# Kernel optimization log

Hardware: AMD Instinct MI355X
Metric: run time of the kernel (lower is better)

Reference implementation:

```python
import jax, jax.numpy as jnp
import numpy as np

N, E = 100000, 1600000
IN, H, Z, C = 64, 128, 64, 2


def _glorot(key, fan_in, fan_out):
    s = jnp.sqrt(2.0 / (fan_in + fan_out)).astype(jnp.float32)
    return jax.random.normal(key, (fan_in, fan_out), dtype=jnp.float32) * s


def setup_inputs() -> dict:
    key = jax.random.key(0)
    ks = jax.random.split(key, 16)
    dims = [(IN, H), (H, H), (H, Z), (H, H), (H, Z), (Z, H), (H, H), (H, IN * C)]
    names = ['in', 'mu0', 'mu', 'si0', 'si', 'z', 'd0', 'out']
    inp = {
        'x': jax.random.normal(ks[0], (N, IN), dtype=jnp.float32),
        'eps': jax.random.normal(ks[1], (N, Z), dtype=jnp.float32),
        'edge_index': jax.random.randint(ks[2], (2, E), 0, N, dtype=jnp.int64),
    }
    for i, (nm, (fi, fo)) in enumerate(zip(names, dims)):
        inp[f'w_{nm}'] = _glorot(ks[3 + i], fi, fo)
        inp[f'b_{nm}'] = jnp.zeros((fo,), dtype=jnp.float32)
    return inp


def _gcn(x, W, b, src, dst, dinv):
    # PyG GCNConv: symmetric normalization with self-loops.
    h = x @ W                                      # [N, d_out]
    norm = (dinv[src] * dinv[dst])[:, None]        # [E, 1]
    agg = jax.ops.segment_sum(h[src] * norm, dst, num_segments=N)
    agg = agg + h * (dinv * dinv)[:, None]         # self-loop term (norm = 1/deg)
    return agg + b


def reference(x, edge_index, eps,
              w_in, b_in, w_mu0, b_mu0, w_mu, b_mu,
              w_si0, b_si0, w_si, b_si,
              w_z, b_z, w_d0, b_d0, w_out, b_out):
    src, dst = edge_index[0], edge_index[1]
    deg = jax.ops.segment_sum(jnp.ones((E,), jnp.float32), dst, num_segments=N) + 1.0
    dinv = jax.lax.rsqrt(deg)
    # encode
    h = jax.nn.relu(_gcn(x, w_in, b_in, src, dst, dinv))
    mu = jax.nn.relu(_gcn(h, w_mu0, b_mu0, src, dst, dinv))
    mu = jax.nn.relu(_gcn(mu, w_mu, b_mu, src, dst, dinv))
    si = jax.nn.relu(_gcn(h, w_si0, b_si0, src, dst, dinv))
    si = jax.nn.sigmoid(_gcn(si, w_si, b_si, src, dst, dinv))
    # reparameterize
    z = mu + si * eps
    # decode (first decoder layer has no activation, per the original forward)
    r = _gcn(z, w_z, b_z, src, dst, dinv)
    r = jax.nn.relu(_gcn(r, w_d0, b_d0, src, dst, dinv))
    logits = _gcn(r, w_out, b_out, src, dst, dinv)   # [N, IN*C]
    logits = logits.reshape(-1, C)                   # [N*IN, C]
    return logits, mu, si
```

## Files before the change

### kernel.cpp

```cpp
#include <hip/hip_runtime.h>


typedef short bf16x8 __attribute__((ext_vector_type(8)));
typedef float f32x4 __attribute__((ext_vector_type(4)));

__device__ __forceinline__ ushort f2bf(float f) {
    uint x = __float_as_uint(f);
    uint r = x + 0x7FFFu + ((x >> 16) & 1u);
    return (ushort)(r >> 16);
}
__device__ __forceinline__ float bf2f(ushort h) {
    return __uint_as_float(((uint)h) << 16);
}
__device__ __forceinline__ float dot2bf(uint a, uint b, float c) {
    float d;
    asm("v_dot2_f32_bf16 %0, %1, %2, %3" : "=v"(d) : "v"(a), "v"(b), "v"(c));
    return d;
}

__global__ __launch_bounds__(1024) void counts_kernel(const int* __restrict__ dst,
        int* __restrict__ deg, int* __restrict__ bc0, int E, int NB, int shift) {
    __shared__ int h[8192];
    for (int j = threadIdx.x; j < NB; j += 1024) h[j] = 0;
    __syncthreads();
    int stride = gridDim.x * 1024;
    for (int i = blockIdx.x * 1024 + threadIdx.x; i < E; i += stride) {
        int d = dst[i];
        atomicAdd(&deg[d], 1);
        atomicAdd(&h[d >> shift], 1);
    }
    __syncthreads();
    for (int j = threadIdx.x; j < NB; j += 1024) {
        int v = h[j];
        if (v) atomicAdd(&bc0[j], v);
    }
}

__global__ void dinv_kernel(const int* __restrict__ deg, float* __restrict__ dinv, int N) {
    int i = blockIdx.x * blockDim.x + threadIdx.x;
    if (i < N) dinv[i] = rsqrtf((float)(deg[i] + 1));
}

__global__ __launch_bounds__(1024) void scan_block_kernel(const int* __restrict__ in,
                                                          int* __restrict__ out,
                                                          int* __restrict__ bsum, int n) {
    __shared__ int s[1024];
    int i = blockIdx.x * 1024 + threadIdx.x;
    int v = (i < n) ? in[i] : 0;
    s[threadIdx.x] = v;
    __syncthreads();
    for (int off = 1; off < 1024; off <<= 1) {
        int t = (threadIdx.x >= off) ? s[threadIdx.x - off] : 0;
        __syncthreads();
        s[threadIdx.x] += t;
        __syncthreads();
    }
    if (i < n) out[i] = s[threadIdx.x] - v;
    if (threadIdx.x == 1023) bsum[blockIdx.x] = s[1023];
}

__global__ __launch_bounds__(1024) void scan_partials_kernel(int* __restrict__ bsum, int nb) {
    __shared__ int s[1024];
    int v = (threadIdx.x < nb) ? bsum[threadIdx.x] : 0;
    s[threadIdx.x] = v;
    __syncthreads();
    for (int off = 1; off < 1024; off <<= 1) {
        int t = (threadIdx.x >= off) ? s[threadIdx.x - off] : 0;
        __syncthreads();
        s[threadIdx.x] += t;
        __syncthreads();
    }
    if (threadIdx.x < nb) bsum[threadIdx.x] = s[threadIdx.x] - v;
}

__global__ __launch_bounds__(1024) void scan_add_kernel(int* __restrict__ arr,
                                                        const int* __restrict__ bsum, int n, int total) {
    int i = blockIdx.x * 1024 + threadIdx.x;
    if (i < n) arr[i] += bsum[blockIdx.x];
    if (i == 0) arr[n] = total;
}

__global__ void scatter_kernel(const int* __restrict__ src, const int* __restrict__ dst,
                               const int* __restrict__ bin_start, int* __restrict__ bc1,
                               int2* __restrict__ ebuf, int E, int shift) {
    int i = blockIdx.x * blockDim.x + threadIdx.x;
    if (i < E) {
        int d = dst[i];
        int b = d >> shift;
        int pos = bin_start[b] + atomicAdd(&bc1[b], 1);
        ebuf[pos] = make_int2(src[i], d);
    }
}

__global__ void place2_kernel(const int2* __restrict__ ebuf, const int* __restrict__ row_start,
                              int* __restrict__ cnt, int2* __restrict__ csr,
                              const float* __restrict__ dinv, int E) {
    int i = blockIdx.x * blockDim.x + threadIdx.x;
    if (i < E) {
        int2 e = ebuf[i];
        int pos = row_start[e.y] + atomicAdd(&cnt[e.y], 1);
        csr[pos] = make_int2(e.x, (int)(uint)f2bf(dinv[e.x] * dinv[e.y]));
    }
}

__global__ void rowsum_kernel(const int2* __restrict__ csr, const int* __restrict__ row_start,
                              const float* __restrict__ dinv, float* __restrict__ cvec, int N) {
    int j = blockIdx.x * blockDim.x + threadIdx.x;
    if (j >= N) return;
    float s = dinv[j] * dinv[j];
    int b = row_start[j], e = row_start[j + 1];
    for (int k = b; k < e; ++k) s += bf2f((ushort)((uint)csr[k].y & 0xFFFFu));
    cvec[j] = s;
}

__global__ void wcpack_kernel(const float* __restrict__ w_z, const float* __restrict__ b_z,
                              const float* __restrict__ w_d0,
                              ushort* __restrict__ P_wc, float* __restrict__ bzw) {
    int o = blockIdx.x * 256 + threadIdx.x;
    if (o >= 65 * 128) return;
    int i = o >> 7, j = o & 127;
    float s = 0.f;
    for (int k = 0; k < 128; ++k) {
        float a = (i < 64) ? w_z[i * 128 + k] : b_z[k];
        s = fmaf(a, w_d0[k * 128 + j], s);
    }
    if (i < 64) {
        int c = j >> 4, kb = i >> 5, l = ((i >> 3) & 3) * 16 + (j & 15), e = i & 7;
        P_wc[(size_t)((c * 2 + kb) * 64 + l) * 8 + e] = f2bf(s);
    } else bzw[j] = s;
}

__device__ __forceinline__ void pack_one(const float* __restrict__ W, ushort* __restrict__ P,
                                         int KI, int KO, int idx) {
    if (idx >= KI * KO) return;
    int e = idx & 7, l = (idx >> 3) & 63, t = idx >> 9;
    int KB = KI / 32;
    int c = t / KB, kb = t % KB;
    int k = kb * 32 + ((l >> 4) << 3) + e, col = c * 16 + (l & 15);
    P[idx] = f2bf(W[(size_t)k * KO + col]);
}

__global__ void megapack_kernel(const float* w_in, const float* w_mu0, const float* w_si0,
                                const float* w_mu, const float* w_si, const float* w_out,
                                ushort* P_in, ushort* P_mu0, ushort* P_si0,
                                ushort* P_mu, ushort* P_si, ushort* P_out) {
    int b = blockIdx.x, tid = threadIdx.x;
    if (b < 32)       pack_one(w_in,  P_in,  64, 128,  (b - 0)   * 256 + tid);
    else if (b < 96)  pack_one(w_mu0, P_mu0, 128, 128, (b - 32)  * 256 + tid);
    else if (b < 160) pack_one(w_si0, P_si0, 128, 128, (b - 96)  * 256 + tid);
    else if (b < 192) pack_one(w_mu,  P_mu,  128, 64,  (b - 160) * 256 + tid);
    else if (b < 224) pack_one(w_si,  P_si,  128, 64,  (b - 192) * 256 + tid);
    else              pack_one(w_out, P_out, 128, 128, (b - 224) * 256 + tid);
}

__global__ void cvt8_kernel(const float* __restrict__ in, ushort* __restrict__ out, int n8) {
    int i = blockIdx.x * 256 + threadIdx.x;
    if (i >= n8) return;
    float4 a = ((const float4*)in)[i * 2];
    float4 b = ((const float4*)in)[i * 2 + 1];
    bf16x8 o;
    o[0] = (short)f2bf(a.x); o[1] = (short)f2bf(a.y);
    o[2] = (short)f2bf(a.z); o[3] = (short)f2bf(a.w);
    o[4] = (short)f2bf(b.x); o[5] = (short)f2bf(b.y);
    o[6] = (short)f2bf(b.z); o[7] = (short)f2bf(b.w);
    ((bf16x8*)out)[i] = o;
}

template <int W>
__device__ __forceinline__ void gather_pairs(float* acc, const ushort* __restrict__ xb,
        const int2* __restrict__ csr, int node, int beg, int end, int sub, int f8) {
    for (int base = beg; base < end; base += 2 * (64 / (W / 8))) {
        int e0 = base + 2 * sub, e1 = e0 + 1;
        int2 p0 = csr[e0 < end ? e0 : beg];
        int2 p1 = csr[e1 < end ? e1 : beg];
        int s0 = (e0 < end) ? p0.x : node;
        int s1 = (e1 < end) ? p1.x : node;
        uint w0 = (e0 < end) ? (uint)p0.y : 0u;
        uint w1 = (e1 < end) ? (uint)p1.y : 0u;
        uint wpk = __builtin_amdgcn_perm(w1, w0, 0x05040100u);
        uint4 v0 = *(const uint4*)(xb + (size_t)s0 * W + f8 * 8);
        uint4 v1 = *(const uint4*)(xb + (size_t)s1 * W + f8 * 8);
        uint t;
        t = __builtin_amdgcn_perm(v1.x, v0.x, 0x05040100u); acc[0] = dot2bf(t, wpk, acc[0]);
        t = __builtin_amdgcn_perm(v1.x, v0.x, 0x07060302u); acc[1] = dot2bf(t, wpk, acc[1]);
        t = __builtin_amdgcn_perm(v1.y, v0.y, 0x05040100u); acc[2] = dot2bf(t, wpk, acc[2]);
        t = __builtin_amdgcn_perm(v1.y, v0.y, 0x07060302u); acc[3] = dot2bf(t, wpk, acc[3]);
        t = __builtin_amdgcn_perm(v1.z, v0.z, 0x05040100u); acc[4] = dot2bf(t, wpk, acc[4]);
        t = __builtin_amdgcn_perm(v1.z, v0.z, 0x07060302u); acc[5] = dot2bf(t, wpk, acc[5]);
        t = __builtin_amdgcn_perm(v1.w, v0.w, 0x05040100u); acc[6] = dot2bf(t, wpk, acc[6]);
        t = __builtin_amdgcn_perm(v1.w, v0.w, 0x07060302u); acc[7] = dot2bf(t, wpk, acc[7]);
    }
}

template <int W>
__global__ __launch_bounds__(256) void bprop_kernel(const ushort* __restrict__ xb,
        ushort* __restrict__ out, const int* __restrict__ row_start,
        const int2* __restrict__ csr, const float* __restrict__ dinv, int N) {
    constexpr int L = W / 8;
    int wave = threadIdx.x >> 6, lane = threadIdx.x & 63;
    int node = blockIdx.x * 4 + wave;
    if (node >= N) return;
    int sub = lane / L, f8 = lane % L;
    int beg = row_start[node], end = row_start[node + 1];
    float d2 = dinv[node]; d2 *= d2;
    float acc[8] = {};
    gather_pairs<W>(acc, xb, csr, node, beg, end, sub, f8);
    #pragma unroll
    for (int m = L; m < 64; m <<= 1) {
        #pragma unroll
        for (int q = 0; q < 8; ++q) acc[q] += __shfl_xor(acc[q], m);
    }
    if (sub != 0) return;
    bf16x8 sv = *(const bf16x8*)(xb + (size_t)node * W + f8 * 8);
    bf16x8 oz;
    #pragma unroll
    for (int q = 0; q < 8; ++q) oz[q] = (short)f2bf(fmaf(d2, bf2f((ushort)sv[q]), acc[q]));
    *(bf16x8*)(out + (size_t)node * W + f8 * 8) = oz;
}

__global__ __launch_bounds__(256) void mssz_kernel(const ushort* __restrict__ T,
        const int* __restrict__ row_start, const int2* __restrict__ csr,
        const float* __restrict__ dinv, const float* __restrict__ b_mu,
        const float* __restrict__ b_si, const float* __restrict__ eps,
        float* __restrict__ M, float* __restrict__ S, ushort* __restrict__ zb, int N) {
    constexpr int L = 16;
    int wave = threadIdx.x >> 6, lane = threadIdx.x & 63;
    int node = blockIdx.x * 4 + wave;
    if (node >= N) return;
    int sub = lane / L, f8 = lane % L;
    int beg = row_start[node], end = row_start[node + 1];
    float d2 = dinv[node]; d2 *= d2;
    float acc[8] = {};
    gather_pairs<128>(acc, T, csr, node, beg, end, sub, f8);
    #pragma unroll
    for (int m = 16; m < 64; m <<= 1) {
        #pragma unroll
        for (int q = 0; q < 8; ++q) acc[q] += __shfl_xor(acc[q], m);
    }
    if (sub != 0) return;
    bf16x8 sv = *(const bf16x8*)(T + (size_t)node * 128 + f8 * 8);
    #pragma unroll
    for (int q = 0; q < 8; ++q) acc[q] = fmaf(d2, bf2f((ushort)sv[q]), acc[q]);

    bool is_mu = (f8 < 8);
    const float* bp = is_mu ? b_mu : b_si;
    int o = (f8 & 7) * 8;
    float val[8];
    #pragma unroll
    for (int q = 0; q < 8; ++q) {
        float t = acc[q] + bp[o + q];
        val[q] = is_mu ? fmaxf(t, 0.f) : 1.f / (1.f + __expf(-t));
    }
    if (is_mu) {
        *(float4*)&M[(size_t)node * 64 + o]     = make_float4(val[0], val[1], val[2], val[3]);
        *(float4*)&M[(size_t)node * 64 + o + 4] = make_float4(val[4], val[5], val[6], val[7]);
    } else {
        *(float4*)&S[(size_t)node * 64 + o]     = make_float4(val[0], val[1], val[2], val[3]);
        *(float4*)&S[(size_t)node * 64 + o + 4] = make_float4(val[4], val[5], val[6], val[7]);
    }
    float oth[8];
    #pragma unroll
    for (int q = 0; q < 8; ++q) oth[q] = __shfl_xor(val[q], 8);
    if (is_mu) {
        float4 e0v = *(const float4*)&eps[(size_t)node * 64 + o];
        float4 e1v = *(const float4*)&eps[(size_t)node * 64 + o + 4];
        float ev[8] = {e0v.x, e0v.y, e0v.z, e0v.w, e1v.x, e1v.y, e1v.z, e1v.w};
        bf16x8 z;
        #pragma unroll
        for (int q = 0; q < 8; ++q) z[q] = (short)f2bf(fmaf(oth[q], ev[q], val[q]));
        *(bf16x8*)(zb + (size_t)node * 64 + o) = z;
    }
}

template <int KI, int KO, int EPI, int OUT>
__global__ __launch_bounds__(256) void mgemm_kernel(const ushort* __restrict__ Xb,
                                                    const bf16x8* __restrict__ Wp,
                                                    const float* __restrict__ bias,
                                                    const float* __restrict__ bias2,
                                                    const float* __restrict__ cvec,
                                                    void* __restrict__ outp, int ostride, int N) {
    constexpr int KB = KI / 32;
    constexpr int CT = KO / 16;
    constexpr size_t LSB = (OUT == 1) ? (size_t)64 * KO * 4 : (size_t)64 * KO * 2;
    __shared__ __align__(16) char LsRaw[LSB];

    int w = threadIdx.x >> 6, l = threadIdx.x & 63;
    int lr = l & 15, lk = l >> 4;
    int rowbase = blockIdx.x * 64;
    int r0 = rowbase + w * 16;

    int arow = r0 + lr; if (arow > N - 1) arow = N - 1;
    bf16x8 a[KB];
    const ushort* xp = Xb + (size_t)arow * KI + lk * 8;
    #pragma unroll
    for (int kb = 0; kb < KB; ++kb) a[kb] = *(const bf16x8*)(xp + kb * 32);

    float cv[4];
    if constexpr (EPI == 3) {
        #pragma unroll
        for (int r = 0; r < 4; ++r) {
            int rr = r0 + lk * 4 + r;
            cv[r] = cvec[rr < N ? rr : 0];
        }
    }

    #pragma unroll
    for (int c = 0; c < CT; ++c) {
        f32x4 acc = {0.f, 0.f, 0.f, 0.f};
        #pragma unroll
        for (int kb = 0; kb < KB; ++kb)
            acc = __builtin_amdgcn_mfma_f32_16x16x32_bf16(a[kb], Wp[((size_t)c * KB + kb) * 64 + l], acc, 0, 0, 0);
        int col = c * 16 + lr;
        float bv = 0.f, b2v = 0.f;
        if constexpr (EPI >= 1) bv = bias[col];
        if constexpr (EPI == 3) b2v = bias2[col];
        #pragma unroll
        for (int r = 0; r < 4; ++r) {
            float v = acc[r];
            if constexpr (EPI == 1) v += bv;
            if constexpr (EPI == 2) v = fmaxf(v + bv, 0.f);
            if constexpr (EPI == 3) v = fmaxf(v + cv[r] * bv + b2v, 0.f);
            int rl = w * 16 + lk * 4 + r;
            if constexpr (OUT == 0) ((ushort*)LsRaw)[(size_t)rl * KO + col] = f2bf(v);
            else                    ((float*)LsRaw)[(size_t)rl * KO + col] = v;
        }
    }
    __syncthreads();

    if constexpr (OUT == 0) {
        ushort* o = (ushort*)outp;
        constexpr int CH = 64 * KO / 8;
        for (int idx = threadIdx.x; idx < CH; idx += 256) {
            int row = idx / (KO / 8), c8 = idx % (KO / 8);
            if (rowbase + row < N)
                *(bf16x8*)(o + (size_t)(rowbase + row) * ostride + c8 * 8) = ((const bf16x8*)LsRaw)[idx];
        }
    } else {
        float* o = (float*)outp;
        constexpr int CH = 64 * KO / 4;
        for (int idx = threadIdx.x; idx < CH; idx += 256) {
            int row = idx / (KO / 4), c4 = idx % (KO / 4);
            if (rowbase + row < N)
                *(float4*)(o + (size_t)(rowbase + row) * ostride + c4 * 4) = ((const float4*)LsRaw)[idx];
        }
    }
}

extern "C" void kernel_launch(void* const* d_in, const int* in_sizes, int n_in,
                              void* d_out, int out_size, void* d_ws, size_t ws_size,
                              hipStream_t stream) {
    const float* x    = (const float*)d_in[0];
    const float* eps  = (const float*)d_in[1];
    const int*   ei   = (const int*)d_in[2];
    const float* w_in  = (const float*)d_in[3];  const float* b_in  = (const float*)d_in[4];
    const float* w_mu0 = (const float*)d_in[5];  const float* b_mu0 = (const float*)d_in[6];
    const float* w_mu  = (const float*)d_in[7];  const float* b_mu  = (const float*)d_in[8];
    const float* w_si0 = (const float*)d_in[9];  const float* b_si0 = (const float*)d_in[10];
    const float* w_si  = (const float*)d_in[11]; const float* b_si  = (const float*)d_in[12];
    const float* w_z   = (const float*)d_in[13]; const float* b_z   = (const float*)d_in[14];
    const float* w_d0  = (const float*)d_in[15]; const float* b_d0  = (const float*)d_in[16];
    const float* w_out = (const float*)d_in[17]; const float* b_out = (const float*)d_in[18];

    const int N = in_sizes[0] / 64;
    const int E = in_sizes[2] / 2;
    const int* srcI = ei;
    const int* dstI = ei + E;

    int shift = 4;
    while (((N >> shift) + 1) > 8192) shift++;
    const int NB = (N >> shift) + 1;

    auto align = [](size_t v) { return (v + 255) & ~(size_t)255; };
    char* wsp = (char*)d_ws;
    size_t off = 0;
    int*    deg       = (int*)(wsp + off);    size_t deg_off = off; off = align(off + (size_t)N * 4);
    int*    bc0       = (int*)(wsp + off);    off = align(off + (size_t)NB * 4);
    int*    bc1       = (int*)(wsp + off);    off = align(off + (size_t)NB * 4);
    size_t  zero_span = off - deg_off;
    float*  cvec      = (float*)(wsp + off);  off = align(off + (size_t)N * 4);
    int*    row_start = (int*)(wsp + off);    off = align(off + (size_t)(N + 1) * 4);
    int*    bin_start = (int*)(wsp + off);    off = align(off + (size_t)(NB + 1) * 4);
    int*    bsum      = (int*)(wsp + off);    off = align(off + 1024 * 4);
    float*  dinv      = (float*)(wsp + off);  off = align(off + (size_t)N * 4);
    float*  bzw       = (float*)(wsp + off);  off = align(off + 128 * 4);
    ushort* P_in      = (ushort*)(wsp + off); off = align(off + 64 * 128 * 2);
    ushort* P_mu0     = (ushort*)(wsp + off); off = align(off + 128 * 128 * 2);
    ushort* P_si0     = (ushort*)(wsp + off); off = align(off + 128 * 128 * 2);
    ushort* P_mu      = (ushort*)(wsp + off); off = align(off + 128 * 64 * 2);
    ushort* P_si      = (ushort*)(wsp + off); off = align(off + 128 * 64 * 2);
    ushort* P_wc      = (ushort*)(wsp + off); off = align(off + 64 * 128 * 2);
    ushort* P_out     = (ushort*)(wsp + off); off = align(off + 128 * 128 * 2);
    int2*   csr       = (int2*)(wsp + off);   off = align(off + (size_t)E * 8);
    int2*   ebuf      = (int2*)(wsp + off);   off = align(off + (size_t)E * 8);
    ushort* xb        = (ushort*)ebuf;
    ushort* B1        = (ushort*)(wsp + off); off = align(off + (size_t)N * 128 * 2);
    ushort* B1lo = B1;
    ushort* B1hi = B1 + (size_t)N * 64;

    float* Cc = (float*)d_out;
    float* M  = Cc + (size_t)N * 128;
    float* S  = M + (size_t)N * 64;
    ushort* CcLo = (ushort*)Cc;
    ushort* CcHi = (ushort*)(Cc + (size_t)N * 64);
    ushort* Db   = (ushort*)M;

    const int TB = 256;
    hipMemsetAsync(deg, 0, zero_span, stream);
    counts_kernel<<<256, 1024, 0, stream>>>(dstI, deg, bc0, E, NB, shift);
    dinv_kernel<<<(N + TB - 1) / TB, TB, 0, stream>>>(deg, dinv, N);
    int nbN = (N + 1023) / 1024;
    scan_block_kernel<<<nbN, 1024, 0, stream>>>(deg, row_start, bsum, N);
    scan_partials_kernel<<<1, 1024, 0, stream>>>(bsum, nbN);
    scan_add_kernel<<<nbN, 1024, 0, stream>>>(row_start, bsum, N, E);
    int nbB = (NB + 1023) / 1024;
    scan_block_kernel<<<nbB, 1024, 0, stream>>>(bc0, bin_start, bsum, NB);
    scan_partials_kernel<<<1, 1024, 0, stream>>>(bsum, nbB);
    scan_add_kernel<<<nbB, 1024, 0, stream>>>(bin_start, bsum, NB, E);
    hipMemsetAsync(deg, 0, (size_t)N * 4, stream);
    scatter_kernel<<<(E + TB - 1) / TB, TB, 0, stream>>>(srcI, dstI, bin_start, bc1, ebuf, E, shift);
    place2_kernel<<<(E + TB - 1) / TB, TB, 0, stream>>>(ebuf, row_start, deg, csr, dinv, E);
    rowsum_kernel<<<(N + TB - 1) / TB, TB, 0, stream>>>(csr, row_start, dinv, cvec, N);
    wcpack_kernel<<<(65 * 128 + 255) / 256, 256, 0, stream>>>(w_z, b_z, w_d0, P_wc, bzw);
    megapack_kernel<<<288, 256, 0, stream>>>(w_in, w_mu0, w_si0, w_mu, w_si, w_out,
                                             P_in, P_mu0, P_si0, P_mu, P_si, P_out);
    cvt8_kernel<<<((N * 8) + 255) / 256, 256, 0, stream>>>(x, xb, N * 8);

    int PG = (N + 3) / 4;
    int GB = (N + 63) / 64;

    bprop_kernel<64><<<PG, 256, 0, stream>>>(xb, B1lo, row_start, csr, dinv, N);
    mgemm_kernel<64, 128, 2, 0><<<GB, 256, 0, stream>>>(B1lo, (const bf16x8*)P_in, b_in, nullptr, nullptr, CcLo, 128, N);
    bprop_kernel<128><<<PG, 256, 0, stream>>>(CcLo, Db, row_start, csr, dinv, N);
    mgemm_kernel<128, 128, 2, 0><<<GB, 256, 0, stream>>>(Db, (const bf16x8*)P_mu0, b_mu0, nullptr, nullptr, B1, 128, N);
    mgemm_kernel<128, 64, 0, 0><<<GB, 256, 0, stream>>>(B1, (const bf16x8*)P_mu, nullptr, nullptr, nullptr, CcHi, 128, N);
    mgemm_kernel<128, 128, 2, 0><<<GB, 256, 0, stream>>>(Db, (const bf16x8*)P_si0, b_si0, nullptr, nullptr, CcLo, 128, N);
    mgemm_kernel<128, 64, 0, 0><<<GB, 256, 0, stream>>>(CcLo, (const bf16x8*)P_si, nullptr, nullptr, nullptr, CcHi + 64, 128, N);
    mssz_kernel<<<PG, 256, 0, stream>>>(CcHi, row_start, csr, dinv, b_mu, b_si, eps, M, S, B1lo, N);
    bprop_kernel<64><<<PG, 256, 0, stream>>>(B1lo, B1hi, row_start, csr, dinv, N);
    bprop_kernel<64><<<PG, 256, 0, stream>>>(B1hi, xb, row_start, csr, dinv, N);
    mgemm_kernel<64, 128, 3, 0><<<GB, 256, 0, stream>>>(xb, (const bf16x8*)P_wc, bzw, b_d0, cvec, CcLo, 128, N);
    bprop_kernel<128><<<PG, 256, 0, stream>>>(CcLo, B1, row_start, csr, dinv, N);
    mgemm_kernel<128, 128, 1, 1><<<GB, 256, 0, stream>>>(B1, (const bf16x8*)P_out, b_out, nullptr, nullptr, Cc, 128, N);
}
```

Before: 673.6 us.

## Fuse encoder mu/sigma GEMM chain into one kernel and deepen gather loads

```diff
diff --git a/kernel.cpp b/kernel.cpp
--- a/kernel.cpp
+++ b/kernel.cpp
@@ -166,33 +166,47 @@
     ((bf16x8*)out)[i] = o;
 }
 
-template <int W>
+template <int W, int DEPTH>
 __device__ __forceinline__ void gather_pairs(float* acc, const ushort* __restrict__ xb,
         const int2* __restrict__ csr, int node, int beg, int end, int sub, int f8) {
-    for (int base = beg; base < end; base += 2 * (64 / (W / 8))) {
-        int e0 = base + 2 * sub, e1 = e0 + 1;
-        int2 p0 = csr[e0 < end ? e0 : beg];
-        int2 p1 = csr[e1 < end ? e1 : beg];
-        int s0 = (e0 < end) ? p0.x : node;
-        int s1 = (e1 < end) ? p1.x : node;
-        uint w0 = (e0 < end) ? (uint)p0.y : 0u;
-        uint w1 = (e1 < end) ? (uint)p1.y : 0u;
-        uint wpk = __builtin_amdgcn_perm(w1, w0, 0x05040100u);
-        uint4 v0 = *(const uint4*)(xb + (size_t)s0 * W + f8 * 8);
-        uint4 v1 = *(const uint4*)(xb + (size_t)s1 * W + f8 * 8);
-        uint t;
-        t = __builtin_amdgcn_perm(v1.x, v0.x, 0x05040100u); acc[0] = dot2bf(t, wpk, acc[0]);
-        t = __builtin_amdgcn_perm(v1.x, v0.x, 0x07060302u); acc[1] = dot2bf(t, wpk, acc[1]);
-        t = __builtin_amdgcn_perm(v1.y, v0.y, 0x05040100u); acc[2] = dot2bf(t, wpk, acc[2]);
-        t = __builtin_amdgcn_perm(v1.y, v0.y, 0x07060302u); acc[3] = dot2bf(t, wpk, acc[3]);
-        t = __builtin_amdgcn_perm(v1.z, v0.z, 0x05040100u); acc[4] = dot2bf(t, wpk, acc[4]);
-        t = __builtin_amdgcn_perm(v1.z, v0.z, 0x07060302u); acc[5] = dot2bf(t, wpk, acc[5]);
-        t = __builtin_amdgcn_perm(v1.w, v0.w, 0x05040100u); acc[6] = dot2bf(t, wpk, acc[6]);
-        t = __builtin_amdgcn_perm(v1.w, v0.w, 0x07060302u); acc[7] = dot2bf(t, wpk, acc[7]);
-    }
-}
-
-template <int W>
+    constexpr int SLOTS = 64 / (W / 8);
+    for (int base = beg; base < end; base += 2 * SLOTS * DEPTH) {
+        int sidx[DEPTH][2];
+        uint wv[DEPTH][2];
+        #pragma unroll
+        for (int d = 0; d < DEPTH; ++d) {
+            int e0 = base + 2 * (sub + SLOTS * d), e1 = e0 + 1;
+            int2 p0 = csr[e0 < end ? e0 : beg];
+            int2 p1 = csr[e1 < end ? e1 : beg];
+            sidx[d][0] = (e0 < end) ? p0.x : node;
+            sidx[d][1] = (e1 < end) ? p1.x : node;
+            wv[d][0] = (e0 < end) ? (uint)p0.y : 0u;
+            wv[d][1] = (e1 < end) ? (uint)p1.y : 0u;
+        }
+        uint4 rv[DEPTH][2];
+        #pragma unroll
+        for (int d = 0; d < DEPTH; ++d) {
+            rv[d][0] = *(const uint4*)(xb + (size_t)sidx[d][0] * W + f8 * 8);
+            rv[d][1] = *(const uint4*)(xb + (size_t)sidx[d][1] * W + f8 * 8);
+        }
+        #pragma unroll
+        for (int d = 0; d < DEPTH; ++d) {
+            uint wpk = __builtin_amdgcn_perm(wv[d][1], wv[d][0], 0x05040100u);
+            uint4 v0 = rv[d][0], v1 = rv[d][1];
+            uint t;
+            t = __builtin_amdgcn_perm(v1.x, v0.x, 0x05040100u); acc[0] = dot2bf(t, wpk, acc[0]);
+            t = __builtin_amdgcn_perm(v1.x, v0.x, 0x07060302u); acc[1] = dot2bf(t, wpk, acc[1]);
+            t = __builtin_amdgcn_perm(v1.y, v0.y, 0x05040100u); acc[2] = dot2bf(t, wpk, acc[2]);
+            t = __builtin_amdgcn_perm(v1.y, v0.y, 0x07060302u); acc[3] = dot2bf(t, wpk, acc[3]);
+            t = __builtin_amdgcn_perm(v1.z, v0.z, 0x05040100u); acc[4] = dot2bf(t, wpk, acc[4]);
+            t = __builtin_amdgcn_perm(v1.z, v0.z, 0x07060302u); acc[5] = dot2bf(t, wpk, acc[5]);
+            t = __builtin_amdgcn_perm(v1.w, v0.w, 0x05040100u); acc[6] = dot2bf(t, wpk, acc[6]);
+            t = __builtin_amdgcn_perm(v1.w, v0.w, 0x07060302u); acc[7] = dot2bf(t, wpk, acc[7]);
+        }
+    }
+}
+
+template <int W, int DEPTH>
 __global__ __launch_bounds__(256) void bprop_kernel(const ushort* __restrict__ xb,
         ushort* __restrict__ out, const int* __restrict__ row_start,
         const int2* __restrict__ csr, const float* __restrict__ dinv, int N) {
@@ -204,7 +218,7 @@
     int beg = row_start[node], end = row_start[node + 1];
     float d2 = dinv[node]; d2 *= d2;
     float acc[8] = {};
-    gather_pairs<W>(acc, xb, csr, node, beg, end, sub, f8);
+    gather_pairs<W, DEPTH>(acc, xb, csr, node, beg, end, sub, f8);
     #pragma unroll
     for (int m = L; m < 64; m <<= 1) {
         #pragma unroll
@@ -231,7 +245,7 @@
     int beg = row_start[node], end = row_start[node + 1];
     float d2 = dinv[node]; d2 *= d2;
     float acc[8] = {};
-    gather_pairs<128>(acc, T, csr, node, beg, end, sub, f8);
+    gather_pairs<128, 2>(acc, T, csr, node, beg, end, sub, f8);
     #pragma unroll
     for (int m = 16; m < 64; m <<= 1) {
         #pragma unroll
@@ -269,6 +283,94 @@
         #pragma unroll
         for (int q = 0; q < 8; ++q) z[q] = (short)f2bf(fmaf(oth[q], ev[q], val[q]));
         *(bf16x8*)(zb + (size_t)node * 64 + o) = z;
+    }
+}
+
+__global__ __launch_bounds__(256) void encgemm_kernel(const ushort* __restrict__ PH,
+        const bf16x8* __restrict__ Pmu0, const float* __restrict__ b_mu0,
+        const bf16x8* __restrict__ Pmu,
+        const bf16x8* __restrict__ Psi0, const float* __restrict__ b_si0,
+        const bf16x8* __restrict__ Psi,
+        ushort* __restrict__ T, int N) {
+    constexpr int STR = 136;
+    __shared__ __align__(16) ushort Ls[64 * STR];
+    int w = threadIdx.x >> 6, l = threadIdx.x & 63;
+    int lr = l & 15, lk = l >> 4;
+    int rowbase = blockIdx.x * 64;
+    int arow = rowbase + w * 16 + lr; if (arow > N - 1) arow = N - 1;
+
+    bf16x8 aph[4];
+    const ushort* pp = PH + (size_t)arow * 128 + lk * 8;
+    #pragma unroll
+    for (int kb = 0; kb < 4; ++kb) aph[kb] = *(const bf16x8*)(pp + kb * 32);
+
+    int crow0 = w * 16 + lk * 4;
+    int afrow = w * 16 + lr;
+
+    #pragma unroll
+    for (int c = 0; c < 8; ++c) {
+        f32x4 acc = {0.f, 0.f, 0.f, 0.f};
+        #pragma unroll
+        for (int kb = 0; kb < 4; ++kb)
+            acc = __builtin_amdgcn_mfma_f32_16x16x32_bf16(aph[kb], Pmu0[((size_t)c * 4 + kb) * 64 + l], acc, 0, 0, 0);
+        float bv = b_mu0[c * 16 + lr];
+        #pragma unroll
+        for (int r = 0; r < 4; ++r)
+            Ls[(crow0 + r) * STR + c * 16 + lr] = f2bf(fmaxf(acc[r] + bv, 0.f));
+    }
+    __syncthreads();
+    bf16x8 am[4];
+    #pragma unroll
+    for (int kb = 0; kb < 4; ++kb) am[kb] = *(const bf16x8*)&Ls[afrow * STR + kb * 32 + lk * 8];
+    f32x4 tmu[4];
+    #pragma unroll
+    for (int c = 0; c < 4; ++c) {
+        f32x4 acc = {0.f, 0.f, 0.f, 0.f};
+        #pragma unroll
+        for (int kb = 0; kb < 4; ++kb)
+            acc = __builtin_amdgcn_mfma_f32_16x16x32_bf16(am[kb], Pmu[((size_t)c * 4 + kb) * 64 + l], acc, 0, 0, 0);
+        tmu[c] = acc;
+    }
+    __syncthreads();
+    #pragma unroll
+    for (int c = 0; c < 8; ++c) {
+        f32x4 acc = {0.f, 0.f, 0.f, 0.f};
+        #pragma unroll
+        for (int kb = 0; kb < 4; ++kb)
+            acc = __builtin_amdgcn_mfma_f32_16x16x32_bf16(aph[kb], Psi0[((size_t)c * 4 + kb) * 64 + l], acc, 0, 0, 0);
+        float bv = b_si0[c * 16 + lr];
+        #pragma unroll
+        for (int r = 0; r < 4; ++r)
+            Ls[(crow0 + r) * STR + c * 16 + lr] = f2bf(fmaxf(acc[r] + bv, 0.f));
+    }
+    __syncthreads();
+    #pragma unroll
+    for (int kb = 0; kb < 4; ++kb) am[kb] = *(const bf16x8*)&Ls[afrow * STR + kb * 32 + lk * 8];
+    f32x4 tsi[4];
+    #pragma unroll
+    for (int c = 0; c < 4; ++c) {
+        f32x4 acc = {0.f, 0.f, 0.f, 0.f};
+        #pragma unroll
+        for (int kb = 0; kb < 4; ++kb)
+            acc = __builtin_amdgcn_mfma_f32_16x16x32_bf16(am[kb], Psi[((size_t)c * 4 + kb) * 64 + l], acc, 0, 0, 0);
+        tsi[c] = acc;
+    }
+    __syncthreads();
+    #pragma unroll
+    for (int c = 0; c < 4; ++c) {
+        #pragma unroll
+        for (int r = 0; r < 4; ++r) {
+            Ls[(crow0 + r) * STR + c * 16 + lr]      = f2bf(tmu[c][r]);
+            Ls[(crow0 + r) * STR + 64 + c * 16 + lr] = f2bf(tsi[c][r]);
+        }
+    }
+    __syncthreads();
+    for (int idx = threadIdx.x; idx < 64 * 16; idx += 256) {
+        int row = idx >> 4, c8 = idx & 15;
+        if (rowbase + row < N) {
+            bf16x8 vv = *(const bf16x8*)&Ls[row * STR + c8 * 8];
+            *(bf16x8*)(T + (size_t)(rowbase + row) * 128 + c8 * 8) = vv;
+        }
     }
 }
 
@@ -428,17 +530,17 @@
     int PG = (N + 3) / 4;
     int GB = (N + 63) / 64;
 
-    bprop_kernel<64><<<PG, 256, 0, stream>>>(xb, B1lo, row_start, csr, dinv, N);
+    bprop_kernel<64, 1><<<PG, 256, 0, stream>>>(xb, B1lo, row_start, csr, dinv, N);
     mgemm_kernel<64, 128, 2, 0><<<GB, 256, 0, stream>>>(B1lo, (const bf16x8*)P_in, b_in, nullptr, nullptr, CcLo, 128, N);
-    bprop_kernel<128><<<PG, 256, 0, stream>>>(CcLo, Db, row_start, csr, dinv, N);
-    mgemm_kernel<128, 128, 2, 0><<<GB, 256, 0, stream>>>(Db, (const bf16x8*)P_mu0, b_mu0, nullptr, nullptr, B1, 128, N);
-    mgemm_kernel<128, 64, 0, 0><<<GB, 256, 0, stream>>>(B1, (const bf16x8*)P_mu, nullptr, nullptr, nullptr, CcHi, 128, N);
-    mgemm_kernel<128, 128, 2, 0><<<GB, 256, 0, stream>>>(Db, (const bf16x8*)P_si0, b_si0, nullptr, nullptr, CcLo, 128, N);
-    mgemm_kernel<128, 64, 0, 0><<<GB, 256, 0, stream>>>(CcLo, (const bf16x8*)P_si, nullptr, nullptr, nullptr, CcHi + 64, 128, N);
+    bprop_kernel<128, 2><<<PG, 256, 0, stream>>>(CcLo, Db, row_start, csr, dinv, N);
+    encgemm_kernel<<<GB, 256, 0, stream>>>(Db,
+                                           (const bf16x8*)P_mu0, b_mu0, (const bf16x8*)P_mu,
+                                           (const bf16x8*)P_si0, b_si0, (const bf16x8*)P_si,
+                                           CcHi, N);
     mssz_kernel<<<PG, 256, 0, stream>>>(CcHi, row_start, csr, dinv, b_mu, b_si, eps, M, S, B1lo, N);
-    bprop_kernel<64><<<PG, 256, 0, stream>>>(B1lo, B1hi, row_start, csr, dinv, N);
-    bprop_kernel<64><<<PG, 256, 0, stream>>>(B1hi, xb, row_start, csr, dinv, N);
+    bprop_kernel<64, 1><<<PG, 256, 0, stream>>>(B1lo, B1hi, row_start, csr, dinv, N);
+    bprop_kernel<64, 1><<<PG, 256, 0, stream>>>(B1hi, xb, row_start, csr, dinv, N);
     mgemm_kernel<64, 128, 3, 0><<<GB, 256, 0, stream>>>(xb, (const bf16x8*)P_wc, bzw, b_d0, cvec, CcLo, 128, N);
-    bprop_kernel<128><<<PG, 256, 0, stream>>>(CcLo, B1, row_start, csr, dinv, N);
+    bprop_kernel<128, 2><<<PG, 256, 0, stream>>>(CcLo, B1, row_start, csr, dinv, N);
     mgemm_kernel<128, 128, 1, 1><<<GB, 256, 0, stream>>>(B1, (const bf16x8*)P_out, b_out, nullptr, nullptr, Cc, 128, N);
 }
```

Result: faster. 660.1 us (-2.0%).
